# Kernel tuning notes

Hardware: AMD Instinct MI355X
Metric: run time of the kernel (lower is better)

The kernel has to match this reference:

```python
import jax, jax.numpy as jnp
import numpy as np


def silu(v):
    return v * jax.nn.sigmoid(v)


def setup_inputs() -> dict:
    key = jax.random.key(0)
    ks = jax.random.split(key, 12)
    B, L, Din, H, Dout = 8, 2048, 64, 256, 64
    d_model, d_state, d_conv, expand = 512, 16, 4, 2
    d_inner = expand * d_model
    dt_rank = d_model // 16  # ceil(512/16) = 32
    s = 0.02

    def n(k, shape):
        return jax.random.normal(k, shape, jnp.float32) * s

    return {
        "x": jax.random.normal(ks[0], (B, L, Din), jnp.float32),
        "enc_w1": n(ks[1], (H, Din)), "enc_b1": jnp.zeros((H,), jnp.float32),
        "enc_w2": n(ks[2], (d_model, H)), "enc_b2": jnp.zeros((d_model,), jnp.float32),
        "in_proj_w": n(ks[3], (2 * d_inner, d_model)),
        "conv_w": n(ks[4], (d_inner, 1, d_conv)), "conv_b": jnp.zeros((d_inner,), jnp.float32),
        "x_proj_w": n(ks[5], (dt_rank + 2 * d_state, d_inner)),
        "dt_proj_w": n(ks[6], (d_inner, dt_rank)), "dt_proj_b": jnp.zeros((d_inner,), jnp.float32),
        "A_log": jnp.log(jnp.broadcast_to(jnp.arange(1, d_state + 1, dtype=jnp.float32), (d_inner, d_state))),
        "D_param": jnp.ones((d_inner,), jnp.float32),
        "out_proj_w": n(ks[7], (d_model, d_inner)),
        "dec_w1": n(ks[8], (H, d_model)), "dec_b1": jnp.zeros((H,), jnp.float32),
        "dec_w2": n(ks[9], (Dout, H)), "dec_b2": jnp.zeros((Dout,), jnp.float32),
    }


def reference(x, enc_w1, enc_b1, enc_w2, enc_b2, in_proj_w, conv_w, conv_b,
              x_proj_w, dt_proj_w, dt_proj_b, A_log, D_param, out_proj_w,
              dec_w1, dec_b1, dec_w2, dec_b2):
    # ---- encoder MLP ----
    h = jax.nn.relu(x @ enc_w1.T + enc_b1)
    u = h @ enc_w2.T + enc_b2  # [B, L, d_model]
    B, L, _ = u.shape
    d_inner = in_proj_w.shape[0] // 2
    d_state = A_log.shape[1]
    dt_rank = dt_proj_w.shape[1]
    d_conv = conv_w.shape[-1]

    # ---- Mamba: input projection + gate split ----
    xz = u @ in_proj_w.T                       # [B, L, 2*d_inner]
    xm, z = jnp.split(xz, 2, axis=-1)

    # ---- causal depthwise conv1d ----
    xc = jnp.transpose(xm, (0, 2, 1))          # [B, d_inner, L]
    xc = jax.lax.conv_general_dilated(xc, conv_w, (1,), [(d_conv - 1, 0)],
                                      feature_group_count=d_inner)
    xc = xc + conv_b[None, :, None]
    xm = silu(jnp.transpose(xc, (0, 2, 1)))    # [B, L, d_inner]

    # ---- input-dependent SSM params ----
    dbl = xm @ x_proj_w.T                      # [B, L, dt_rank + 2*d_state]
    dt = dbl[..., :dt_rank]
    Bm = dbl[..., dt_rank:dt_rank + d_state]   # [B, L, d_state]
    Cm = dbl[..., dt_rank + d_state:]          # [B, L, d_state]
    delta = jax.nn.softplus(dt @ dt_proj_w.T + dt_proj_b)  # [B, L, d_inner]
    A = -jnp.exp(A_log)                        # [d_inner, d_state]

    # ---- selective scan over sequence ----
    def step(hs, inp):
        x_t, d_t, B_t, C_t = inp               # [B,d_inner],[B,d_inner],[B,d_state],[B,d_state]
        dA = jnp.exp(d_t[:, :, None] * A)      # [B, d_inner, d_state]
        hs = dA * hs + (d_t * x_t)[:, :, None] * B_t[:, None, :]
        y_t = jnp.einsum('bds,bs->bd', hs, C_t)
        return hs, y_t

    h0 = jnp.zeros((B, d_inner, d_state), xm.dtype)
    xs = (jnp.swapaxes(xm, 0, 1), jnp.swapaxes(delta, 0, 1),
          jnp.swapaxes(Bm, 0, 1), jnp.swapaxes(Cm, 0, 1))
    _, ys = jax.lax.scan(step, h0, xs)         # ys: [L, B, d_inner]

    y = jnp.swapaxes(ys, 0, 1) + xm * D_param  # skip term
    y = y * silu(z)                            # gate
    out = y @ out_proj_w.T                     # [B, L, d_model]

    # ---- decoder MLP ----
    h2 = jax.nn.relu(out @ dec_w1.T + dec_b1)
    return h2 @ dec_w2.T + dec_b2              # [B, L, output_dim]
```

## Files before the change

### kernel.cpp

```cpp
#include <hip/hip_runtime.h>
#include <hip/hip_bf16.h>

typedef __attribute__((ext_vector_type(8))) short bf16x8;
typedef __attribute__((ext_vector_type(4))) float f32x4;
typedef __attribute__((ext_vector_type(4))) unsigned short u16x4;
typedef __hip_bfloat16 bf16;

#define DEV __device__ __forceinline__
DEV float sigmoidf_(float x) { return 1.0f / (1.0f + __expf(-x)); }
DEV float bf2f(bf16 v) { return __bfloat162float(v); }
DEV bf16  f2bf(float v) { return __float2bfloat16(v); }

typedef const __attribute__((address_space(1))) void* gptr_t;
typedef __attribute__((address_space(3))) void* lptr_t;

template<int N> DEV void waitcnt_vm() {
    if constexpr (N == 0) asm volatile("s_waitcnt vmcnt(0)" ::: "memory");
    else if constexpr (N == 2) asm volatile("s_waitcnt vmcnt(2)" ::: "memory");
    else if constexpr (N == 3) asm volatile("s_waitcnt vmcnt(3)" ::: "memory");
    else asm volatile("s_waitcnt vmcnt(4)" ::: "memory");
}

template<int BM, int BN, int ACT, int OUTBF>
__global__ __launch_bounds__(256)
void gemm_mfma(const bf16* __restrict__ A, int lda,
               const bf16* __restrict__ W, int ldw,
               const float* __restrict__ bias,
               void* __restrict__ Cp, int ldc, int K)
{
    constexpr int BK = 32;
    constexpr int WMS = BM / 2, WNS = BN / 2;
    constexpr int FM = WMS / 16, FN = WNS / 16;
    constexpr int AITER = (BM * BK) / (256 * 8);
    constexpr int BITER = (BN * BK) / (256 * 8);
    constexpr int NLD = AITER + BITER;
    constexpr int BUFB = (BM + BN) * BK * 2;

    __shared__ __align__(16) char smem[2 * BUFB];

    const int tid = threadIdx.x;
    const int lane = tid & 63;
    const int wid = tid >> 6;
    const int wm = wid >> 1, wn = wid & 1;
    const long m0 = (long)blockIdx.y * BM;
    const long n0 = (long)blockIdx.x * BN;

    f32x4 acc[FM][FN] = {};

    long aoff[AITER];
#pragma unroll
    for (int it = 0; it < AITER; ++it) {
        int q = it * 256 + tid;
        int r = q >> 2;
        aoff[it] = (long)(m0 + r) * lda * 2 + (((q & 3) * 16) ^ ((r & 3) << 4));
    }
    long boff[BITER];
#pragma unroll
    for (int it = 0; it < BITER; ++it) {
        int q = it * 256 + tid;
        int r = q >> 2;
        boff[it] = (long)(n0 + r) * ldw * 2 + (((q & 3) * 16) ^ ((r & 3) << 4));
    }

    const char* Ac = (const char*)A;
    const char* Wc = (const char*)W;

#pragma unroll
    for (int it = 0; it < AITER; ++it)
        __builtin_amdgcn_global_load_lds((gptr_t)(Ac + aoff[it]),
            (lptr_t)(smem + (it * 256 + wid * 64) * 16), 16, 0, 0);
#pragma unroll
    for (int it = 0; it < BITER; ++it)
        __builtin_amdgcn_global_load_lds((gptr_t)(Wc + boff[it]),
            (lptr_t)(smem + BM * BK * 2 + (it * 256 + wid * 64) * 16), 16, 0, 0);

    const int NK = K / BK;
    const int fr = lane & 15, fq = lane >> 4;
    const int swz = (fr & 3) << 4;
    int cur = 0;

    for (int ks = 0; ks < NK; ++ks) {
        if (ks + 1 < NK) {
            const long k2 = (long)(ks + 1) * BK * 2;
            char* dst = smem + (cur ^ 1) * BUFB;
#pragma unroll
            for (int it = 0; it < AITER; ++it)
                __builtin_amdgcn_global_load_lds((gptr_t)(Ac + aoff[it] + k2),
                    (lptr_t)(dst + (it * 256 + wid * 64) * 16), 16, 0, 0);
#pragma unroll
            for (int it = 0; it < BITER; ++it)
                __builtin_amdgcn_global_load_lds((gptr_t)(Wc + boff[it] + k2),
                    (lptr_t)(dst + BM * BK * 2 + (it * 256 + wid * 64) * 16), 16, 0, 0);
            waitcnt_vm<NLD>();
        } else {
            waitcnt_vm<0>();
        }
        __builtin_amdgcn_s_barrier();
        __builtin_amdgcn_sched_barrier(0);

        const char* base = smem + cur * BUFB;
        bf16x8 av[FM], bv[FN];
#pragma unroll
        for (int fm = 0; fm < FM; ++fm) {
            int ra = wm * WMS + fm * 16 + fr;
            av[fm] = *(const bf16x8*)(base + ra * 64 + ((fq * 16) ^ swz));
        }
#pragma unroll
        for (int fn = 0; fn < FN; ++fn) {
            int rb = wn * WNS + fn * 16 + fr;
            bv[fn] = *(const bf16x8*)(base + BM * BK * 2 + rb * 64 + ((fq * 16) ^ swz));
        }
#pragma unroll
        for (int fm = 0; fm < FM; ++fm)
#pragma unroll
            for (int fn = 0; fn < FN; ++fn)
                acc[fm][fn] = __builtin_amdgcn_mfma_f32_16x16x32_bf16(
                    av[fm], bv[fn], acc[fm][fn], 0, 0, 0);

        asm volatile("s_waitcnt lgkmcnt(0)" ::: "memory");
        __builtin_amdgcn_sched_barrier(0);
        __builtin_amdgcn_s_barrier();
        cur ^= 1;
    }

    float bcol[FN];
#pragma unroll
    for (int fn = 0; fn < FN; ++fn)
        bcol[fn] = bias ? bias[n0 + wn * WNS + fn * 16 + fr] : 0.0f;

    if constexpr (OUTBF) {
        constexpr int CST = BN + 8;
        bf16* ct = (bf16*)smem;
        for (int mh = 0; mh < BM / 64; ++mh) {
            __syncthreads();
            if (BM == 64 || wm == mh) {
#pragma unroll
                for (int fm = 0; fm < FM; ++fm) {
                    int lr0 = (BM == 64 ? wm * WMS : 0) + fm * 16 + fq * 4;
#pragma unroll
                    for (int fn = 0; fn < FN; ++fn) {
                        int lc = wn * WNS + fn * 16 + fr;
#pragma unroll
                        for (int r = 0; r < 4; ++r) {
                            float v = acc[fm][fn][r] + bcol[fn];
                            if (ACT == 1) v = fmaxf(v, 0.0f);
                            else if (ACT == 2)
                                v = fmaxf(v, 0.0f) + __logf(1.0f + __expf(-fabsf(v)));
                            ct[(lr0 + r) * CST + lc] = f2bf(v);
                        }
                    }
                }
            }
            __syncthreads();
            constexpr int GPR = BN / 8;
#pragma unroll
            for (int it = 0; it < (64 * GPR) / 256; ++it) {
                int idx = it * 256 + tid;
                int row = idx / GPR, cg = idx % GPR;
                bf16x8 v8 = *(const bf16x8*)&ct[row * CST + cg * 8];
                *(bf16x8*)((bf16*)Cp + (size_t)(m0 + mh * 64 + row) * ldc
                           + n0 + cg * 8) = v8;
            }
        }
    } else {
#pragma unroll
        for (int fn = 0; fn < FN; ++fn) {
            long col = n0 + wn * WNS + fn * 16 + fr;
#pragma unroll
            for (int fm = 0; fm < FM; ++fm) {
                long row0 = m0 + wm * WMS + fm * 16 + fq * 4;
#pragma unroll
                for (int r = 0; r < 4; ++r) {
                    float v = acc[fm][fn][r] + bcol[fn];
                    if (ACT == 1) v = fmaxf(v, 0.0f);
                    ((float*)Cp)[(size_t)(row0 + r) * ldc + col] = v;
                }
            }
        }
    }
}

struct CastJobs {
    const float* src[9];
    bf16* dst[9];
    int n[9];
};

__global__ __launch_bounds__(256)
void cast_bf16_kernel(CastJobs J)
{
    const int seg = blockIdx.y;
    const f32x4* s = (const f32x4*)J.src[seg];
    u16x4* d = (u16x4*)J.dst[seg];
    const int n4 = J.n[seg] >> 2;
    for (int i = blockIdx.x * 256 + threadIdx.x; i < n4; i += gridDim.x * 256) {
        f32x4 v = s[i];
        u16x4 o;
#pragma unroll
        for (int j = 0; j < 4; ++j) {
            bf16 b = f2bf(v[j]);
            o[j] = *(unsigned short*)&b;
        }
        d[i] = o;
    }
}

#define DSTATE 16
#define CHUNK 16

__global__ __launch_bounds__(256)
void conv_silu_kernel(const bf16* __restrict__ xmr, const float* __restrict__ cw,
                      const float* __restrict__ cb, bf16* __restrict__ xms, int L)
{
    const int NCc = L / 32;
    const int c = blockIdx.x % NCc;
    const int b = blockIdx.x / NCc;
    const int d = blockIdx.y * 256 + threadIdx.x;

    const float w0 = cw[d * 4 + 0], w1 = cw[d * 4 + 1];
    const float w2 = cw[d * 4 + 2], w3 = cw[d * 4 + 3];
    const float bb = cb[d];

    const int t0 = c * 32;
    float x0 = 0.f, x1 = 0.f, x2 = 0.f;
    if (t0 >= 3) {
        x0 = bf2f(xmr[(size_t)(b * L + t0 - 3) * 1024 + d]);
        x1 = bf2f(xmr[(size_t)(b * L + t0 - 2) * 1024 + d]);
        x2 = bf2f(xmr[(size_t)(b * L + t0 - 1) * 1024 + d]);
    }
    for (int t = t0; t < t0 + 32; ++t) {
        float x3 = bf2f(xmr[(size_t)(b * L + t) * 1024 + d]);
        float v = fmaf(w0, x0, fmaf(w1, x1, fmaf(w2, x2, fmaf(w3, x3, bb))));
        xms[(size_t)(b * L + t) * 1024 + d] = f2bf(v * sigmoidf_(v));
        x0 = x1; x1 = x2; x2 = x3;
    }
}

DEV bool load_A(const float* __restrict__ A_log, int d, float* As_)
{
    bool fastA = true;
#pragma unroll
    for (int s = 0; s < DSTATE; ++s) {
        As_[s] = -__expf(A_log[(size_t)d * DSTATE + s]);
        fastA = fastA && (fabsf(As_[s] + (float)(s + 1)) <= 1e-4f * (s + 1));
    }
    return fastA;
}

DEV void powa(float r, float* a)
{
    float r2 = r * r;
    float r4 = r2 * r2;
    float r8 = r4 * r4;
    float r3 = r2 * r;
    a[0] = r;       a[1] = r2;      a[2] = r3;      a[3] = r4;
    a[4] = r4 * r;  a[5] = r4 * r2; a[6] = r4 * r3; a[7] = r8;
    a[8] = r8 * r;  a[9] = r8 * r2; a[10] = r8 * r3; a[11] = r8 * r4;
    a[12] = a[11] * r; a[13] = a[11] * r2; a[14] = a[11] * r3; a[15] = r8 * r8;
}

__global__ __launch_bounds__(256)
void scan_pass1(const bf16* __restrict__ delta, const bf16* __restrict__ xms,
                const bf16* __restrict__ dblb, const float* __restrict__ A_log,
                bf16* __restrict__ P, bf16* __restrict__ S, int L)
{
    const int NC = L / CHUNK;
    const int c = blockIdx.x % NC;
    const int b = blockIdx.x / NC;
    const int d = blockIdx.y * 256 + threadIdx.x;

    __shared__ float Bsh[CHUNK][DSTATE];
    {
        int t = threadIdx.x >> 4, s = threadIdx.x & 15;
        Bsh[t][s] = bf2f(dblb[(size_t)(b * L + c * CHUNK + t) * 64 + 32 + s]);
    }
    __syncthreads();

    float As_[DSTATE];
    const bool fastA = load_A(A_log, d, As_);

    float h[DSTATE], p[DSTATE];
#pragma unroll
    for (int s = 0; s < DSTATE; ++s) { h[s] = 0.f; p[s] = 1.f; }

    const size_t rb = (size_t)(b * L + c * CHUNK);
    float de_n = bf2f(delta[rb * 1024 + d]);
    float x_n  = bf2f(xms[rb * 1024 + d]);

    if (fastA) {
#pragma unroll 4
        for (int t = 0; t < CHUNK; ++t) {
            float de = de_n, x = x_n;
            if (t + 1 < CHUNK) {
                de_n = bf2f(delta[(rb + t + 1) * 1024 + d]);
                x_n  = bf2f(xms[(rb + t + 1) * 1024 + d]);
            }
            float dx = de * x;
            float r = __expf(-de);
            float a[DSTATE];
            powa(r, a);
#pragma unroll
            for (int s = 0; s < DSTATE; ++s) {
                h[s] = fmaf(a[s], h[s], dx * Bsh[t][s]);
                p[s] *= a[s];
            }
        }
    } else {
#pragma unroll 4
        for (int t = 0; t < CHUNK; ++t) {
            float de = de_n, x = x_n;
            if (t + 1 < CHUNK) {
                de_n = bf2f(delta[(rb + t + 1) * 1024 + d]);
                x_n  = bf2f(xms[(rb + t + 1) * 1024 + d]);
            }
            float dx = de * x;
#pragma unroll
            for (int s = 0; s < DSTATE; ++s) {
                float dA = __expf(de * As_[s]);
                h[s] = fmaf(dA, h[s], dx * Bsh[t][s]);
                p[s] *= dA;
            }
        }
    }
#pragma unroll
    for (int s = 0; s < DSTATE; ++s) {
        size_t o = ((size_t)(b * NC + c) * DSTATE + s) * 1024 + d;
        P[o] = f2bf(p[s]);
        S[o] = f2bf(h[s]);
    }
}

__global__ __launch_bounds__(256)
void scan_pass2(const bf16* P, const bf16* __restrict__ S, bf16* Hinit, int NC)
{
    int g = blockIdx.x * 256 + threadIdx.x;
    int d = g & 1023;
    int s = (g >> 10) & 15;
    int b = g >> 14;
    const size_t cs = (size_t)DSTATE * 1024;
    size_t o = ((size_t)(b * NC) * DSTATE + s) * 1024 + d;
    float h = 0.f;
    for (int c0 = 0; c0 < NC; c0 += 8) {
        float pv[8], sv[8];
#pragma unroll
        for (int j = 0; j < 8; ++j) {
            pv[j] = bf2f(P[o + j * cs]);
            sv[j] = bf2f(S[o + j * cs]);
        }
#pragma unroll
        for (int j = 0; j < 8; ++j) {
            Hinit[o + j * cs] = f2bf(h);
            h = fmaf(pv[j], h, sv[j]);
        }
        o += 8 * cs;
    }
}

__global__ __launch_bounds__(256)
void scan_pass3(const bf16* delta, const bf16* __restrict__ xms,
                const bf16* __restrict__ dblb, const float* __restrict__ A_log,
                const bf16* __restrict__ Hinit, const float* __restrict__ Dp,
                const bf16* __restrict__ zb, bf16* Y, int L)
{
    const int NC = L / CHUNK;
    const int c = blockIdx.x % NC;
    const int b = blockIdx.x / NC;
    const int d = blockIdx.y * 256 + threadIdx.x;

    __shared__ float Bsh[CHUNK][DSTATE];
    __shared__ float Csh[CHUNK][DSTATE];
    {
        int t = threadIdx.x >> 4, s = threadIdx.x & 15;
        size_t base = (size_t)(b * L + c * CHUNK + t) * 64;
        Bsh[t][s] = bf2f(dblb[base + 32 + s]);
        Csh[t][s] = bf2f(dblb[base + 48 + s]);
    }
    __syncthreads();

    float As_[DSTATE];
    const bool fastA = load_A(A_log, d, As_);

    float h[DSTATE];
#pragma unroll
    for (int s = 0; s < DSTATE; ++s)
        h[s] = bf2f(Hinit[((size_t)(b * NC + c) * DSTATE + s) * 1024 + d]);

    const float Dd = Dp[d];
    const size_t rb = (size_t)(b * L + c * CHUNK);
    float de_n = bf2f(delta[rb * 1024 + d]);
    float x_n  = bf2f(xms[rb * 1024 + d]);
    float z_n  = bf2f(zb[rb * 1024 + d]);

    if (fastA) {
#pragma unroll 4
        for (int t = 0; t < CHUNK; ++t) {
            float de = de_n, x = x_n, z = z_n;
            if (t + 1 < CHUNK) {
                de_n = bf2f(delta[(rb + t + 1) * 1024 + d]);
                x_n  = bf2f(xms[(rb + t + 1) * 1024 + d]);
                z_n  = bf2f(zb[(rb + t + 1) * 1024 + d]);
            }
            float dx = de * x;
            float r = __expf(-de);
            float a[DSTATE];
            powa(r, a);
            float y0 = 0.f, y1 = 0.f;
#pragma unroll
            for (int s = 0; s < DSTATE; s += 2) {
                h[s] = fmaf(a[s], h[s], dx * Bsh[t][s]);
                y0 = fmaf(h[s], Csh[t][s], y0);
                h[s+1] = fmaf(a[s+1], h[s+1], dx * Bsh[t][s+1]);
                y1 = fmaf(h[s+1], Csh[t][s+1], y1);
            }
            float y = y0 + y1 + x * Dd;
            Y[(rb + t) * 1024 + d] = f2bf(y * (z * sigmoidf_(z)));
        }
    } else {
#pragma unroll 4
        for (int t = 0; t < CHUNK; ++t) {
            float de = de_n, x = x_n, z = z_n;
            if (t + 1 < CHUNK) {
                de_n = bf2f(delta[(rb + t + 1) * 1024 + d]);
                x_n  = bf2f(xms[(rb + t + 1) * 1024 + d]);
                z_n  = bf2f(zb[(rb + t + 1) * 1024 + d]);
            }
            float dx = de * x;
            float y0 = 0.f, y1 = 0.f;
#pragma unroll
            for (int s = 0; s < DSTATE; s += 2) {
                float dA0 = __expf(de * As_[s]);
                float dA1 = __expf(de * As_[s+1]);
                h[s] = fmaf(dA0, h[s], dx * Bsh[t][s]);
                y0 = fmaf(h[s], Csh[t][s], y0);
                h[s+1] = fmaf(dA1, h[s+1], dx * Bsh[t][s+1]);
                y1 = fmaf(h[s+1], Csh[t][s+1], y1);
            }
            float y = y0 + y1 + x * Dd;
            Y[(rb + t) * 1024 + d] = f2bf(y * (z * sigmoidf_(z)));
        }
    }
}


extern "C" void kernel_launch(void* const* d_in, const int* in_sizes, int n_in,
                              void* d_out, int out_size, void* d_ws, size_t ws_size,
                              hipStream_t stream)
{
    (void)in_sizes; (void)n_in; (void)out_size;

    const float* x         = (const float*)d_in[0];
    const float* enc_w1    = (const float*)d_in[1];
    const float* enc_b1    = (const float*)d_in[2];
    const float* enc_w2    = (const float*)d_in[3];
    const float* enc_b2    = (const float*)d_in[4];
    const float* in_proj_w = (const float*)d_in[5];
    const float* conv_w    = (const float*)d_in[6];
    const float* conv_b    = (const float*)d_in[7];
    const float* x_proj_w  = (const float*)d_in[8];
    const float* dt_proj_w = (const float*)d_in[9];
    const float* dt_proj_b = (const float*)d_in[10];
    const float* A_log     = (const float*)d_in[11];
    const float* D_param   = (const float*)d_in[12];
    const float* out_proj_w= (const float*)d_in[13];
    const float* dec_w1    = (const float*)d_in[14];
    const float* dec_b1    = (const float*)d_in[15];
    const float* dec_w2    = (const float*)d_in[16];
    const float* dec_b2    = (const float*)d_in[17];
    float* out = (float*)d_out;

    const int L = 2048, NC = L / CHUNK;

    bf16* wb = (bf16*)d_ws;
    size_t off = 0;
    bf16* w_enc1 = wb + off; off += 16384;
    bf16* w_enc2 = wb + off; off += 131072;
    bf16* w_inpj = wb + off; off += 1048576;
    bf16* w_xprj = wb + off; off += 65536;
    bf16* w_dtpj = wb + off; off += 32768;
    bf16* w_outp = wb + off; off += 524288;
    bf16* w_dec1 = wb + off; off += 131072;
    bf16* w_dec2 = wb + off; off += 16384;
    bf16* xbf    = wb + off; off += 1048576;
    const size_t fixedB = off * 2;

    const size_t PER_ROW = 11904;
    int SPLIT = 8;
    if      (fixedB + (size_t)16384 * PER_ROW <= ws_size) SPLIT = 1;
    else if (fixedB + (size_t) 8192 * PER_ROW <= ws_size) SPLIT = 2;
    else if (fixedB + (size_t) 4096 * PER_ROW <= ws_size) SPLIT = 4;

    const int NB = 8 / SPLIT;
    const int MR = NB * L;

    char* pb = (char*)d_ws + fixedB;
    bf16* hbf   = (bf16*)pb;
    bf16* ubf   = hbf   + (size_t)MR * 256;
    bf16* slot3 = ubf   + (size_t)MR * 512;
    bf16* zbf   = slot3 + (size_t)MR * 1024;
    bf16* xms   = zbf   + (size_t)MR * 1024;
    bf16* dblb  = xms   + (size_t)MR * 1024;
    bf16* Pb    = dblb  + (size_t)MR * 64;
    bf16* Sb    = Pb    + (size_t)MR * 1024;

    CastJobs J;
    J.src[0] = enc_w1;     J.dst[0] = w_enc1; J.n[0] = 16384;
    J.src[1] = enc_w2;     J.dst[1] = w_enc2; J.n[1] = 131072;
    J.src[2] = in_proj_w;  J.dst[2] = w_inpj; J.n[2] = 1048576;
    J.src[3] = x_proj_w;   J.dst[3] = w_xprj; J.n[3] = 65536;
    J.src[4] = dt_proj_w;  J.dst[4] = w_dtpj; J.n[4] = 32768;
    J.src[5] = out_proj_w; J.dst[5] = w_outp; J.n[5] = 524288;
    J.src[6] = dec_w1;     J.dst[6] = w_dec1; J.n[6] = 131072;
    J.src[7] = dec_w2;     J.dst[7] = w_dec2; J.n[7] = 16384;
    J.src[8] = x;          J.dst[8] = xbf;    J.n[8] = 1048576;
    cast_bf16_kernel<<<dim3(128, 9), 256, 0, stream>>>(J);

    dim3 blk(256);
    for (int p = 0; p < SPLIT; ++p) {
        const bf16* xp  = xbf + (size_t)p * MR * 64;
        float*     outp = out + (size_t)p * MR * 64;

        gemm_mfma<64,128,1,1><<<dim3(2, MR/64), blk, 0, stream>>>(
            xp, 64, w_enc1, 64, enc_b1, hbf, 256, 64);
        gemm_mfma<128,128,0,1><<<dim3(4, MR/128), blk, 0, stream>>>(
            hbf, 256, w_enc2, 256, enc_b2, ubf, 512, 256);
        gemm_mfma<128,128,0,1><<<dim3(8, MR/128), blk, 0, stream>>>(
            ubf, 512, w_inpj, 512, nullptr, slot3, 1024, 512);
        gemm_mfma<128,128,0,1><<<dim3(8, MR/128), blk, 0, stream>>>(
            ubf, 512, w_inpj + (size_t)1024 * 512, 512, nullptr, zbf, 1024, 512);
        conv_silu_kernel<<<dim3(NB * (L/32), 4), blk, 0, stream>>>(
            slot3, conv_w, conv_b, xms, L);
        gemm_mfma<64,64,0,1><<<dim3(1, MR/64), blk, 0, stream>>>(
            xms, 1024, w_xprj, 1024, nullptr, dblb, 64, 1024);
        gemm_mfma<128,128,2,1><<<dim3(8, MR/128), blk, 0, stream>>>(
            dblb, 64, w_dtpj, 32, dt_proj_b, slot3, 1024, 32);
        scan_pass1<<<dim3(NB * NC, 4), blk, 0, stream>>>(
            slot3, xms, dblb, A_log, Pb, Sb, L);
        scan_pass2<<<dim3(NB * 64), blk, 0, stream>>>(Pb, Sb, Pb, NC);
        scan_pass3<<<dim3(NB * NC, 4), blk, 0, stream>>>(
            slot3, xms, dblb, A_log, Pb, D_param, zbf, slot3 , L);
        gemm_mfma<128,128,0,1><<<dim3(4, MR/128), blk, 0, stream>>>(
            slot3, 1024, w_outp, 1024, nullptr, ubf, 512, 1024);
        gemm_mfma<64,128,1,1><<<dim3(2, MR/64), blk, 0, stream>>>(
            ubf, 512, w_dec1, 512, dec_b1, hbf, 256, 512);
        gemm_mfma<64,64,0,0><<<dim3(1, MR/64), blk, 0, stream>>>(
            hbf, 256, w_dec2, 256, dec_b2, outp, 64, 256);
    }
}
```

Baseline: 368.7 us.

## Compute local scan output in pass1 and correct with decayed carry in pass3

Pass1 now computes the chunk-local scan output (including the D skip term) and writes it in place over xms. Pass3 no longer recomputes the recurrence; it only propagates the carried-in state through cumulative decay and adds its C-projection. The chunk decay product is derived from the summed delta via powa, and SiLU(z) is fused into the z projection GEMM epilogue. CHUNK grows to 32 and the workspace per row shrinks. The cost is extra stores in pass1 and a dependency on xms being overwritten.

```diff
diff --git a/kernel.cpp b/kernel.cpp
--- a/kernel.cpp
+++ b/kernel.cpp
@@ -7,9 +7,9 @@
 typedef __hip_bfloat16 bf16;
 
 #define DEV __device__ __forceinline__
-DEV float sigmoidf_(float x) { return 1.0f / (1.0f + __expf(-x)); }
 DEV float bf2f(bf16 v) { return __bfloat162float(v); }
 DEV bf16  f2bf(float v) { return __float2bfloat16(v); }
+DEV float sigmoidf_(float x) { return __builtin_amdgcn_rcpf(1.0f + __expf(-x)); }
 
 typedef const __attribute__((address_space(1))) void* gptr_t;
 typedef __attribute__((address_space(3))) void* lptr_t;
@@ -146,6 +146,8 @@
                             if (ACT == 1) v = fmaxf(v, 0.0f);
                             else if (ACT == 2)
                                 v = fmaxf(v, 0.0f) + __logf(1.0f + __expf(-fabsf(v)));
+                            else if (ACT == 3)
+                                v = v * sigmoidf_(v);
                             ct[(lr0 + r) * CST + lc] = f2bf(v);
                         }
                     }
@@ -206,7 +208,7 @@
 }
 
 #define DSTATE 16
-#define CHUNK 16
+#define CHUNK 32
 
 __global__ __launch_bounds__(256)
 void conv_silu_kernel(const bf16* __restrict__ xmr, const float* __restrict__ cw,
@@ -250,9 +252,9 @@
 DEV void powa(float r, float* a)
 {
     float r2 = r * r;
+    float r3 = r2 * r;
     float r4 = r2 * r2;
     float r8 = r4 * r4;
-    float r3 = r2 * r;
     a[0] = r;       a[1] = r2;      a[2] = r3;      a[3] = r4;
     a[4] = r4 * r;  a[5] = r4 * r2; a[6] = r4 * r3; a[7] = r8;
     a[8] = r8 * r;  a[9] = r8 * r2; a[10] = r8 * r3; a[11] = r8 * r4;
@@ -260,8 +262,9 @@
 }
 
 __global__ __launch_bounds__(256)
-void scan_pass1(const bf16* __restrict__ delta, const bf16* __restrict__ xms,
+void scan_pass1(const bf16* __restrict__ delta, bf16* xms ,
                 const bf16* __restrict__ dblb, const float* __restrict__ A_log,
+                const float* __restrict__ Dp,
                 bf16* __restrict__ P, bf16* __restrict__ S, int L)
 {
     const int NC = L / CHUNK;
@@ -270,63 +273,80 @@
     const int d = blockIdx.y * 256 + threadIdx.x;
 
     __shared__ float Bsh[CHUNK][DSTATE];
-    {
-        int t = threadIdx.x >> 4, s = threadIdx.x & 15;
-        Bsh[t][s] = bf2f(dblb[(size_t)(b * L + c * CHUNK + t) * 64 + 32 + s]);
+    __shared__ float Csh[CHUNK][DSTATE];
+#pragma unroll
+    for (int it = 0; it < CHUNK * DSTATE / 256; ++it) {
+        int idx = threadIdx.x + it * 256;
+        int t = idx >> 4, s = idx & 15;
+        size_t base = (size_t)(b * L + c * CHUNK + t) * 64;
+        Bsh[t][s] = bf2f(dblb[base + 32 + s]);
+        Csh[t][s] = bf2f(dblb[base + 48 + s]);
     }
     __syncthreads();
 
     float As_[DSTATE];
     const bool fastA = load_A(A_log, d, As_);
-
-    float h[DSTATE], p[DSTATE];
-#pragma unroll
-    for (int s = 0; s < DSTATE; ++s) { h[s] = 0.f; p[s] = 1.f; }
+    const float Dd = Dp[d];
+
+    float h[DSTATE];
+#pragma unroll
+    for (int s = 0; s < DSTATE; ++s) h[s] = 0.f;
 
     const size_t rb = (size_t)(b * L + c * CHUNK);
-    float de_n = bf2f(delta[rb * 1024 + d]);
-    float x_n  = bf2f(xms[rb * 1024 + d]);
 
     if (fastA) {
-#pragma unroll 4
+        float sumd = 0.f;
         for (int t = 0; t < CHUNK; ++t) {
-            float de = de_n, x = x_n;
-            if (t + 1 < CHUNK) {
-                de_n = bf2f(delta[(rb + t + 1) * 1024 + d]);
-                x_n  = bf2f(xms[(rb + t + 1) * 1024 + d]);
-            }
+            size_t g = (rb + t) * 1024 + d;
+            float de = bf2f(delta[g]);
+            float x  = bf2f(xms[g]);
             float dx = de * x;
             float r = __expf(-de);
             float a[DSTATE];
             powa(r, a);
+            sumd += de;
+            float yl = x * Dd;
 #pragma unroll
             for (int s = 0; s < DSTATE; ++s) {
                 h[s] = fmaf(a[s], h[s], dx * Bsh[t][s]);
-                p[s] *= a[s];
-            }
+                yl = fmaf(h[s], Csh[t][s], yl);
+            }
+            xms[g] = f2bf(yl);
+        }
+        float Rc = __expf(-sumd);
+        float pa[DSTATE];
+        powa(Rc, pa);
+#pragma unroll
+        for (int s = 0; s < DSTATE; ++s) {
+            size_t o = ((size_t)(b * NC + c) * DSTATE + s) * 1024 + d;
+            P[o] = f2bf(pa[s]);
+            S[o] = f2bf(h[s]);
         }
     } else {
-#pragma unroll 4
+        float p[DSTATE];
+#pragma unroll
+        for (int s = 0; s < DSTATE; ++s) p[s] = 1.f;
         for (int t = 0; t < CHUNK; ++t) {
-            float de = de_n, x = x_n;
-            if (t + 1 < CHUNK) {
-                de_n = bf2f(delta[(rb + t + 1) * 1024 + d]);
-                x_n  = bf2f(xms[(rb + t + 1) * 1024 + d]);
-            }
+            size_t g = (rb + t) * 1024 + d;
+            float de = bf2f(delta[g]);
+            float x  = bf2f(xms[g]);
             float dx = de * x;
+            float yl = x * Dd;
 #pragma unroll
             for (int s = 0; s < DSTATE; ++s) {
                 float dA = __expf(de * As_[s]);
                 h[s] = fmaf(dA, h[s], dx * Bsh[t][s]);
                 p[s] *= dA;
-            }
-        }
-    }
-#pragma unroll
-    for (int s = 0; s < DSTATE; ++s) {
-        size_t o = ((size_t)(b * NC + c) * DSTATE + s) * 1024 + d;
-        P[o] = f2bf(p[s]);
-        S[o] = f2bf(h[s]);
+                yl = fmaf(h[s], Csh[t][s], yl);
+            }
+            xms[g] = f2bf(yl);
+        }
+#pragma unroll
+        for (int s = 0; s < DSTATE; ++s) {
+            size_t o = ((size_t)(b * NC + c) * DSTATE + s) * 1024 + d;
+            P[o] = f2bf(p[s]);
+            S[o] = f2bf(h[s]);
+        }
     }
 }
 
@@ -357,86 +377,69 @@
 }
 
 __global__ __launch_bounds__(256)
-void scan_pass3(const bf16* delta, const bf16* __restrict__ xms,
+void scan_pass3(const bf16* delta, const bf16* __restrict__ ylocal,
                 const bf16* __restrict__ dblb, const float* __restrict__ A_log,
-                const bf16* __restrict__ Hinit, const float* __restrict__ Dp,
-                const bf16* __restrict__ zb, bf16* Y, int L)
+                const bf16* __restrict__ Hinit,
+                const bf16* __restrict__ zs, bf16* Y, int L)
 {
     const int NC = L / CHUNK;
     const int c = blockIdx.x % NC;
     const int b = blockIdx.x / NC;
     const int d = blockIdx.y * 256 + threadIdx.x;
 
-    __shared__ float Bsh[CHUNK][DSTATE];
     __shared__ float Csh[CHUNK][DSTATE];
-    {
-        int t = threadIdx.x >> 4, s = threadIdx.x & 15;
-        size_t base = (size_t)(b * L + c * CHUNK + t) * 64;
-        Bsh[t][s] = bf2f(dblb[base + 32 + s]);
-        Csh[t][s] = bf2f(dblb[base + 48 + s]);
+#pragma unroll
+    for (int it = 0; it < CHUNK * DSTATE / 256; ++it) {
+        int idx = threadIdx.x + it * 256;
+        int t = idx >> 4, s = idx & 15;
+        Csh[t][s] = bf2f(dblb[(size_t)(b * L + c * CHUNK + t) * 64 + 48 + s]);
     }
     __syncthreads();
 
     float As_[DSTATE];
     const bool fastA = load_A(A_log, d, As_);
 
-    float h[DSTATE];
+    float w[DSTATE];
 #pragma unroll
     for (int s = 0; s < DSTATE; ++s)
-        h[s] = bf2f(Hinit[((size_t)(b * NC + c) * DSTATE + s) * 1024 + d]);
-
-    const float Dd = Dp[d];
+        w[s] = bf2f(Hinit[((size_t)(b * NC + c) * DSTATE + s) * 1024 + d]);
+
     const size_t rb = (size_t)(b * L + c * CHUNK);
-    float de_n = bf2f(delta[rb * 1024 + d]);
-    float x_n  = bf2f(xms[rb * 1024 + d]);
-    float z_n  = bf2f(zb[rb * 1024 + d]);
 
     if (fastA) {
-#pragma unroll 4
         for (int t = 0; t < CHUNK; ++t) {
-            float de = de_n, x = x_n, z = z_n;
-            if (t + 1 < CHUNK) {
-                de_n = bf2f(delta[(rb + t + 1) * 1024 + d]);
-                x_n  = bf2f(xms[(rb + t + 1) * 1024 + d]);
-                z_n  = bf2f(zb[(rb + t + 1) * 1024 + d]);
-            }
-            float dx = de * x;
+            size_t g = (rb + t) * 1024 + d;
+            float de = bf2f(delta[g]);
+            float yl = bf2f(ylocal[g]);
+            float z  = bf2f(zs[g]);
             float r = __expf(-de);
             float a[DSTATE];
             powa(r, a);
-            float y0 = 0.f, y1 = 0.f;
+            float c0 = 0.f, c1 = 0.f;
 #pragma unroll
             for (int s = 0; s < DSTATE; s += 2) {
-                h[s] = fmaf(a[s], h[s], dx * Bsh[t][s]);
-                y0 = fmaf(h[s], Csh[t][s], y0);
-                h[s+1] = fmaf(a[s+1], h[s+1], dx * Bsh[t][s+1]);
-                y1 = fmaf(h[s+1], Csh[t][s+1], y1);
-            }
-            float y = y0 + y1 + x * Dd;
-            Y[(rb + t) * 1024 + d] = f2bf(y * (z * sigmoidf_(z)));
+                w[s] *= a[s];
+                c0 = fmaf(w[s], Csh[t][s], c0);
+                w[s+1] *= a[s+1];
+                c1 = fmaf(w[s+1], Csh[t][s+1], c1);
+            }
+            Y[g] = f2bf((yl + c0 + c1) * z);
         }
     } else {
-#pragma unroll 4
         for (int t = 0; t < CHUNK; ++t) {
-            float de = de_n, x = x_n, z = z_n;
-            if (t + 1 < CHUNK) {
-                de_n = bf2f(delta[(rb + t + 1) * 1024 + d]);
-                x_n  = bf2f(xms[(rb + t + 1) * 1024 + d]);
-                z_n  = bf2f(zb[(rb + t + 1) * 1024 + d]);
-            }
-            float dx = de * x;
-            float y0 = 0.f, y1 = 0.f;
+            size_t g = (rb + t) * 1024 + d;
+            float de = bf2f(delta[g]);
+            float yl = bf2f(ylocal[g]);
+            float z  = bf2f(zs[g]);
+            float c0 = 0.f, c1 = 0.f;
 #pragma unroll
             for (int s = 0; s < DSTATE; s += 2) {
-                float dA0 = __expf(de * As_[s]);
-                float dA1 = __expf(de * As_[s+1]);
-                h[s] = fmaf(dA0, h[s], dx * Bsh[t][s]);
-                y0 = fmaf(h[s], Csh[t][s], y0);
-                h[s+1] = fmaf(dA1, h[s+1], dx * Bsh[t][s+1]);
-                y1 = fmaf(h[s+1], Csh[t][s+1], y1);
-            }
-            float y = y0 + y1 + x * Dd;
-            Y[(rb + t) * 1024 + d] = f2bf(y * (z * sigmoidf_(z)));
+                w[s]   *= __expf(de * As_[s]);
+                c0 = fmaf(w[s], Csh[t][s], c0);
+                w[s+1] *= __expf(de * As_[s+1]);
+                c1 = fmaf(w[s+1], Csh[t][s+1], c1);
+            }
+            Y[g] = f2bf((yl + c0 + c1) * z);
         }
     }
 }
@@ -483,7 +486,7 @@
     bf16* xbf    = wb + off; off += 1048576;
     const size_t fixedB = off * 2;
 
-    const size_t PER_ROW = 11904;
+    const size_t PER_ROW = 9856;
     int SPLIT = 8;
     if      (fixedB + (size_t)16384 * PER_ROW <= ws_size) SPLIT = 1;
     else if (fixedB + (size_t) 8192 * PER_ROW <= ws_size) SPLIT = 2;
@@ -500,7 +503,7 @@
     bf16* xms   = zbf   + (size_t)MR * 1024;
     bf16* dblb  = xms   + (size_t)MR * 1024;
     bf16* Pb    = dblb  + (size_t)MR * 64;
-    bf16* Sb    = Pb    + (size_t)MR * 1024;
+    bf16* Sb    = Pb    + (size_t)MR * 512;
 
     CastJobs J;
     J.src[0] = enc_w1;     J.dst[0] = w_enc1; J.n[0] = 16384;
@@ -525,7 +528,7 @@
             hbf, 256, w_enc2, 256, enc_b2, ubf, 512, 256);
         gemm_mfma<128,128,0,1><<<dim3(8, MR/128), blk, 0, stream>>>(
             ubf, 512, w_inpj, 512, nullptr, slot3, 1024, 512);
-        gemm_mfma<128,128,0,1><<<dim3(8, MR/128), blk, 0, stream>>>(
+        gemm_mfma<128,128,3,1><<<dim3(8, MR/128), blk, 0, stream>>>(
             ubf, 512, w_inpj + (size_t)1024 * 512, 512, nullptr, zbf, 1024, 512);
         conv_silu_kernel<<<dim3(NB * (L/32), 4), blk, 0, stream>>>(
             slot3, conv_w, conv_b, xms, L);
@@ -534,10 +537,10 @@
         gemm_mfma<128,128,2,1><<<dim3(8, MR/128), blk, 0, stream>>>(
             dblb, 64, w_dtpj, 32, dt_proj_b, slot3, 1024, 32);
         scan_pass1<<<dim3(NB * NC, 4), blk, 0, stream>>>(
-            slot3, xms, dblb, A_log, Pb, Sb, L);
+            slot3, xms, dblb, A_log, D_param, Pb, Sb, L);
         scan_pass2<<<dim3(NB * 64), blk, 0, stream>>>(Pb, Sb, Pb, NC);
         scan_pass3<<<dim3(NB * NC, 4), blk, 0, stream>>>(
-            slot3, xms, dblb, A_log, Pb, D_param, zbf, slot3 , L);
+            slot3, xms, dblb, A_log, Pb, zbf, slot3 , L);
         gemm_mfma<128,128,0,1><<<dim3(4, MR/128), blk, 0, stream>>>(
             slot3, 1024, w_outp, 1024, nullptr, ubf, 512, 1024);
         gemm_mfma<64,128,1,1><<<dim3(2, MR/64), blk, 0, stream>>>(
```

Result: faster. 349.8 us (-5.1%).
